# Kernel tuning notes

Hardware: AMD Instinct MI355X
Metric: run time of the kernel (lower is better)

Reference implementation:

```python
import jax, jax.numpy as jnp
import numpy as np

VOCAB = 200000
EDIM = 256
R = 16


def setup_inputs() -> dict:
    key = jax.random.key(0)
    k0, k1, k2 = jax.random.split(key, 3)
    x = jax.random.randint(k0, (4096, 50), 0, VOCAB)
    # TR cores: core0 (r1, num_embeddings, r0), core1 (r0, embedding_dim, r1)
    core0 = jax.random.normal(k1, (R, VOCAB, R), dtype=jnp.float32)
    core1 = jax.random.normal(k2, (R, EDIM, R), dtype=jnp.float32)
    return {"x": x, "core0": core0, "core1": core1}


def reference(x, core0, core1):
    # tr_to_tensor for 2 cores: weight[i, j] = trace(core0[:, i, :] @ core1[:, j, :])
    # core0: (a=r1, i=vocab, b=r0), core1: (b=r0, j=edim, a=r1)
    weight = jnp.einsum('aib,bja->ij', core0, core1)  # [vocab, edim]
    return weight[x]  # gather: [batch, hist, edim]
```

## Files before the change

### kernel.cpp

```cpp
#include <hip/hip_runtime.h>
#include <hip/hip_bf16.h>

#define VOCAB 200000
#define EDIM  256
#define NTILES 12800
#define GRID   512
#define ITERS  25
#define DEPTH  4

typedef __attribute__((ext_vector_type(4))) float  f32x4;
typedef __attribute__((ext_vector_type(4))) int    i32x4;
typedef __attribute__((ext_vector_type(8))) __bf16 bf16x8;

typedef const __attribute__((address_space(1))) unsigned int* gas_u32p;
typedef __attribute__((address_space(3))) unsigned int* las_u32p;

__device__ __forceinline__ __bf16 f2bf(float f) {
    unsigned u = __builtin_bit_cast(unsigned, f);
    u += 0x7FFFu + ((u >> 16) & 1u);
    unsigned short s = (unsigned short)(u >> 16);
    return __builtin_bit_cast(__bf16, s);
}

__global__ void pack_b_kernel(const float* __restrict__ core1, bf16x8* __restrict__ bpk) {
    int t    = blockIdx.x * 256 + threadIdx.x;
    int lane = t & 63;
    int nt   = (t >> 6) & 15;
    int kk   = t >> 10;
    int j     = nt * 16 + (lane & 15);
    int kbase = kk * 32 + ((lane >> 4) * 8);
    bf16x8 v;
#pragma unroll
    for (int e = 0; e < 8; ++e) {
        int k = kbase + e;
        int b = k & 15, a = k >> 4;
        v[e] = f2bf(core1[(b * 256 + j) * 16 + a]);
    }
    bpk[t] = v;
}

__device__ __forceinline__ void issue_gather(const float* __restrict__ core0, int idx,
                                             int kk, char* abuf, int lane) {
    const int q = lane >> 4;
#pragma unroll
    for (int h = 0; h < 2; ++h) {
        int c = kk * 8 + q * 2 + h;
        const float* src = core0 + ((long)(c >> 2) * VOCAB + idx) * 16 + (c & 3) * 4;
        __builtin_amdgcn_global_load_lds((gas_u32p)src,
                                         (las_u32p)(abuf + kk * 2048 + h * 1024), 16, 0, 0);
    }
}

__global__ __launch_bounds__(512, 4) void tr_embed_kernel(
        const int* __restrict__ x, const float* __restrict__ core0,
        const bf16x8* __restrict__ bpk, float* __restrict__ out) {
    __shared__ char lds[DEPTH * 16384 + ITERS * 16 * 4];
    int* const sIdx = (int*)(lds + DEPTH * 16384);
    const int tid  = threadIdx.x;
    const int lane = tid & 63;
    const int wave = tid >> 6;
    const int r    = lane & 15;
    const int q    = lane >> 4;

    bf16x8 B0[8], B1[8];
#pragma unroll
    for (int kk = 0; kk < 8; ++kk) {
        B0[kk] = bpk[(kk * 16 + 2 * wave)     * 64 + lane];
        B1[kk] = bpk[(kk * 16 + 2 * wave + 1) * 64 + lane];
    }

    const int b0 = blockIdx.x;

    for (int j = tid; j < ITERS * 16; j += 512)
        sIdx[j] = x[(b0 + (j >> 4) * GRID) * 16 + (j & 15)];
    __syncthreads();

#pragma unroll
    for (int p = 0; p < 3; ++p)
        issue_gather(core0, sIdx[p * 16 + r], wave, lds + p * 16384, lane);
    asm volatile("s_waitcnt vmcnt(0)" ::: "memory");
    __builtin_amdgcn_s_barrier();

    for (int i = 0; i < ITERS; ++i) {
        const int t = b0 + i * GRID;
        char* cur = lds + (i & 3) * 16384;

        if (i + 3 < ITERS)
            issue_gather(core0, sIdx[(i + 3) * 16 + r], wave,
                         lds + ((i + 3) & 3) * 16384, lane);
        __builtin_amdgcn_sched_barrier(0);

        f32x4 acc0 = {}, acc1 = {};
#pragma unroll
        for (int kk = 0; kk < 8; ++kk) {
            f32x4 lo = *(const f32x4*)(cur + kk * 2048 +        lane * 16);
            f32x4 hi = *(const f32x4*)(cur + kk * 2048 + 1024 + lane * 16);
            int p0, p1, p2, p3;
            asm("v_cvt_pk_bf16_f32 %0, %1, %2" : "=v"(p0) : "v"(lo[0]), "v"(lo[1]));
            asm("v_cvt_pk_bf16_f32 %0, %1, %2" : "=v"(p1) : "v"(lo[2]), "v"(lo[3]));
            asm("v_cvt_pk_bf16_f32 %0, %1, %2" : "=v"(p2) : "v"(hi[0]), "v"(hi[1]));
            asm("v_cvt_pk_bf16_f32 %0, %1, %2" : "=v"(p3) : "v"(hi[2]), "v"(hi[3]));
            i32x4 pk = { p0, p1, p2, p3 };
            bf16x8 af = __builtin_bit_cast(bf16x8, pk);
            acc0 = __builtin_amdgcn_mfma_f32_16x16x32_bf16(af, B0[kk], acc0, 0, 0, 0);
            acc1 = __builtin_amdgcn_mfma_f32_16x16x32_bf16(af, B1[kk], acc1, 0, 0, 0);
        }

        float* ob = out + (long)t * 16 * 256 + (q * 4) * 256 + 2 * wave * 16 + r;
#pragma unroll
        for (int e = 0; e < 4; ++e) {
            ob[e * 256]      = acc0[e];
            ob[e * 256 + 16] = acc1[e];
        }

        asm volatile("s_waitcnt vmcnt(20)" ::: "memory");
        __builtin_amdgcn_s_barrier();
    }
}

extern "C" void kernel_launch(void* const* d_in, const int* in_sizes, int n_in,
                              void* d_out, int out_size, void* d_ws, size_t ws_size,
                              hipStream_t stream) {
    const int*   x     = (const int*)d_in[0];
    const float* core0 = (const float*)d_in[1];
    const float* core1 = (const float*)d_in[2];
    float* out = (float*)d_out;
    bf16x8* bpk = (bf16x8*)d_ws;

    pack_b_kernel<<<32, 256, 0, stream>>>(core1, bpk);
    tr_embed_kernel<<<GRID, 512, 0, stream>>>(x, core0, bpk, out);
}
```

Measured before the change: 117.0 us.

## Repack core0 into bf16 row-contiguous layout before gathering embeddings

After: 143.6 us. 1.23x slower.

```diff
diff --git a/kernel.cpp b/kernel.cpp
--- a/kernel.cpp
+++ b/kernel.cpp
@@ -37,6 +37,96 @@
         v[e] = f2bf(core1[(b * 256 + j) * 16 + a]);
     }
     bpk[t] = v;
+}
+
+__global__ __launch_bounds__(256) void repack_a_kernel(const float* __restrict__ core0,
+                                                       char* __restrict__ abf) {
+    int t = blockIdx.x * 256 + threadIdx.x;
+    int v = t >> 4, a = t & 15;
+    const float* src = core0 + ((long)a * VOCAB + v) * 16;
+    f32x4 s0 = *(const f32x4*)(src);
+    f32x4 s1 = *(const f32x4*)(src + 4);
+    f32x4 s2 = *(const f32x4*)(src + 8);
+    f32x4 s3 = *(const f32x4*)(src + 12);
+    int p[8];
+    asm("v_cvt_pk_bf16_f32 %0, %1, %2" : "=v"(p[0]) : "v"(s0[0]), "v"(s0[1]));
+    asm("v_cvt_pk_bf16_f32 %0, %1, %2" : "=v"(p[1]) : "v"(s0[2]), "v"(s0[3]));
+    asm("v_cvt_pk_bf16_f32 %0, %1, %2" : "=v"(p[2]) : "v"(s1[0]), "v"(s1[1]));
+    asm("v_cvt_pk_bf16_f32 %0, %1, %2" : "=v"(p[3]) : "v"(s1[2]), "v"(s1[3]));
+    asm("v_cvt_pk_bf16_f32 %0, %1, %2" : "=v"(p[4]) : "v"(s2[0]), "v"(s2[1]));
+    asm("v_cvt_pk_bf16_f32 %0, %1, %2" : "=v"(p[5]) : "v"(s2[2]), "v"(s2[3]));
+    asm("v_cvt_pk_bf16_f32 %0, %1, %2" : "=v"(p[6]) : "v"(s3[0]), "v"(s3[1]));
+    asm("v_cvt_pk_bf16_f32 %0, %1, %2" : "=v"(p[7]) : "v"(s3[2]), "v"(s3[3]));
+    i32x4 lo = { p[0], p[1], p[2], p[3] };
+    i32x4 hi = { p[4], p[5], p[6], p[7] };
+    char* dst = abf + (long)v * 512 + a * 32;
+    *(i32x4*)(dst)      = lo;
+    *(i32x4*)(dst + 16) = hi;
+}
+
+__device__ __forceinline__ void issue_gather_bf(const char* __restrict__ abf, int idx,
+                                                int wave, int q, char* slot) {
+    const char* src = abf + (long)idx * 512 + wave * 64 + q * 16;
+    __builtin_amdgcn_global_load_lds((gas_u32p)src, (las_u32p)(slot + wave * 1024), 16, 0, 0);
+}
+
+__global__ __launch_bounds__(512, 4) void tr_embed_bf_kernel(
+        const int* __restrict__ x, const char* __restrict__ abf,
+        const bf16x8* __restrict__ bpk, float* __restrict__ out) {
+    __shared__ char lds[DEPTH * 8192 + ITERS * 16 * 4];
+    int* const sIdx = (int*)(lds + DEPTH * 8192);
+    const int tid  = threadIdx.x;
+    const int lane = tid & 63;
+    const int wave = tid >> 6;
+    const int r    = lane & 15;
+    const int q    = lane >> 4;
+
+    bf16x8 B0[8], B1[8];
+#pragma unroll
+    for (int kk = 0; kk < 8; ++kk) {
+        B0[kk] = bpk[(kk * 16 + 2 * wave)     * 64 + lane];
+        B1[kk] = bpk[(kk * 16 + 2 * wave + 1) * 64 + lane];
+    }
+
+    const int b0 = blockIdx.x;
+
+    for (int j = tid; j < ITERS * 16; j += 512)
+        sIdx[j] = x[(b0 + (j >> 4) * GRID) * 16 + (j & 15)];
+    __syncthreads();
+
+#pragma unroll
+    for (int p = 0; p < 3; ++p)
+        issue_gather_bf(abf, sIdx[p * 16 + r], wave, q, lds + p * 8192);
+    asm volatile("s_waitcnt vmcnt(0)" ::: "memory");
+    __builtin_amdgcn_s_barrier();
+
+    for (int i = 0; i < ITERS; ++i) {
+        const int t = b0 + i * GRID;
+        char* cur = lds + (i & 3) * 8192;
+
+        if (i + 3 < ITERS)
+            issue_gather_bf(abf, sIdx[(i + 3) * 16 + r], wave, q,
+                            lds + ((i + 3) & 3) * 8192);
+        __builtin_amdgcn_sched_barrier(0);
+
+        f32x4 acc0 = {}, acc1 = {};
+#pragma unroll
+        for (int kk = 0; kk < 8; ++kk) {
+            bf16x8 af = *(const bf16x8*)(cur + kk * 1024 + lane * 16);
+            acc0 = __builtin_amdgcn_mfma_f32_16x16x32_bf16(af, B0[kk], acc0, 0, 0, 0);
+            acc1 = __builtin_amdgcn_mfma_f32_16x16x32_bf16(af, B1[kk], acc1, 0, 0, 0);
+        }
+
+        float* ob = out + (long)t * 16 * 256 + (q * 4) * 256 + 2 * wave * 16 + r;
+#pragma unroll
+        for (int e = 0; e < 4; ++e) {
+            ob[e * 256]      = acc0[e];
+            ob[e * 256 + 16] = acc1[e];
+        }
+
+        asm volatile("s_waitcnt vmcnt(24)" ::: "memory");
+        __builtin_amdgcn_s_barrier();
+    }
 }
 
 __device__ __forceinline__ void issue_gather(const float* __restrict__ core0, int idx,
@@ -70,7 +160,6 @@
     }
 
     const int b0 = blockIdx.x;
-
     for (int j = tid; j < ITERS * 16; j += 512)
         sIdx[j] = x[(b0 + (j >> 4) * GRID) * 16 + (j & 15)];
     __syncthreads();
@@ -84,7 +173,6 @@
     for (int i = 0; i < ITERS; ++i) {
         const int t = b0 + i * GRID;
         char* cur = lds + (i & 3) * 16384;
-
         if (i + 3 < ITERS)
             issue_gather(core0, sIdx[(i + 3) * 16 + r], wave,
                          lds + ((i + 3) & 3) * 16384, lane);
@@ -112,7 +200,6 @@
             ob[e * 256]      = acc0[e];
             ob[e * 256 + 16] = acc1[e];
         }
-
         asm volatile("s_waitcnt vmcnt(20)" ::: "memory");
         __builtin_amdgcn_s_barrier();
     }
@@ -126,7 +213,15 @@
     const float* core1 = (const float*)d_in[2];
     float* out = (float*)d_out;
     bf16x8* bpk = (bf16x8*)d_ws;
+    char*   abf = (char*)d_ws + 131072;
+
+    const size_t WS_NEED = 131072 + (size_t)VOCAB * 512;
 
     pack_b_kernel<<<32, 256, 0, stream>>>(core1, bpk);
-    tr_embed_kernel<<<GRID, 512, 0, stream>>>(x, core0, bpk, out);
-}
+    if (ws_size >= WS_NEED) {
+        repack_a_kernel<<<VOCAB * 16 / 256, 256, 0, stream>>>(core0, abf);
+        tr_embed_bf_kernel<<<GRID, 512, 0, stream>>>(x, abf, bpk, out);
+    } else {
+        tr_embed_kernel<<<GRID, 512, 0, stream>>>(x, core0, bpk, out);
+    }
+}
```

## Stage output tile through swizzled LDS for coalesced 16-byte stores, shrink gather pipeline

Applied to the files above, without the earlier changes.

Result: faster. 112.8 us (-3.5%).

```diff
diff --git a/kernel.cpp b/kernel.cpp
--- a/kernel.cpp
+++ b/kernel.cpp
@@ -1,12 +1,11 @@
 #include <hip/hip_runtime.h>
 #include <hip/hip_bf16.h>
 
-#define VOCAB 200000
-#define EDIM  256
+#define VOCAB  200000
 #define NTILES 12800
 #define GRID   512
 #define ITERS  25
-#define DEPTH  4
+#define DEPTH  3
 
 typedef __attribute__((ext_vector_type(4))) float  f32x4;
 typedef __attribute__((ext_vector_type(4))) int    i32x4;
@@ -54,8 +53,10 @@
 __global__ __launch_bounds__(512, 4) void tr_embed_kernel(
         const int* __restrict__ x, const float* __restrict__ core0,
         const bf16x8* __restrict__ bpk, float* __restrict__ out) {
-    __shared__ char lds[DEPTH * 16384 + ITERS * 16 * 4];
-    int* const sIdx = (int*)(lds + DEPTH * 16384);
+    __shared__ char lds[DEPTH * 16384 + 16384 + ITERS * 16 * 4];
+    char* const ldsA = lds;
+    char* const ldsC = lds + DEPTH * 16384;
+    int*  const sIdx = (int*)(lds + DEPTH * 16384 + 16384);
     const int tid  = threadIdx.x;
     const int lane = tid & 63;
     const int wave = tid >> 6;
@@ -76,18 +77,21 @@
     __syncthreads();
 
 #pragma unroll
-    for (int p = 0; p < 3; ++p)
-        issue_gather(core0, sIdx[p * 16 + r], wave, lds + p * 16384, lane);
+    for (int p = 0; p < 2; ++p)
+        issue_gather(core0, sIdx[p * 16 + r], wave, ldsA + p * 16384, lane);
     asm volatile("s_waitcnt vmcnt(0)" ::: "memory");
     __builtin_amdgcn_s_barrier();
+    __builtin_amdgcn_sched_barrier(0);
 
+    int slot = 0;
     for (int i = 0; i < ITERS; ++i) {
         const int t = b0 + i * GRID;
-        char* cur = lds + (i & 3) * 16384;
+        char* cur = ldsA + slot * 16384;
 
-        if (i + 3 < ITERS)
-            issue_gather(core0, sIdx[(i + 3) * 16 + r], wave,
-                         lds + ((i + 3) & 3) * 16384, lane);
+        if (i + 2 < ITERS) {
+            int ns = slot + 2; if (ns >= DEPTH) ns -= DEPTH;
+            issue_gather(core0, sIdx[(i + 2) * 16 + r], wave, ldsA + ns * 16384, lane);
+        }
         __builtin_amdgcn_sched_barrier(0);
 
         f32x4 acc0 = {}, acc1 = {};
@@ -106,15 +110,32 @@
             acc1 = __builtin_amdgcn_mfma_f32_16x16x32_bf16(af, B1[kk], acc1, 0, 0, 0);
         }
 
-        float* ob = out + (long)t * 16 * 256 + (q * 4) * 256 + 2 * wave * 16 + r;
 #pragma unroll
         for (int e = 0; e < 4; ++e) {
-            ob[e * 256]      = acc0[e];
-            ob[e * 256 + 16] = acc1[e];
+            int row = q * 4 + e;
+            int xr  = (row & 7) << 2;
+            *(float*)(ldsC + row * 1024 + (((2 * wave * 16 + r)      ^ xr) << 2)) = acc0[e];
+            *(float*)(ldsC + row * 1024 + (((2 * wave * 16 + 16 + r) ^ xr) << 2)) = acc1[e];
+        }
+        asm volatile("s_waitcnt lgkmcnt(0)" ::: "memory");
+        __builtin_amdgcn_sched_barrier(0);
+        __builtin_amdgcn_s_barrier();
+        __builtin_amdgcn_sched_barrier(0);
+
+        {
+            int r0w = 2 * wave, r1w = 2 * wave + 1;
+            f32x4 v0 = *(const f32x4*)(ldsC + r0w * 1024 + (((lane * 4) ^ ((r0w & 7) << 2)) << 2));
+            f32x4 v1 = *(const f32x4*)(ldsC + r1w * 1024 + (((lane * 4) ^ ((r1w & 7) << 2)) << 2));
+            float* ob = out + ((long)t * 16 + r0w) * 256;
+            *((f32x4*)ob + lane)         = v0;
+            *((f32x4*)(ob + 256) + lane) = v1;
         }
 
-        asm volatile("s_waitcnt vmcnt(20)" ::: "memory");
+        asm volatile("s_waitcnt vmcnt(6)" ::: "memory");
         __builtin_amdgcn_s_barrier();
+        __builtin_amdgcn_sched_barrier(0);
+
+        slot = (slot == DEPTH - 1) ? 0 : slot + 1;
     }
 }
 
```
